# Performance work log

Measured on AMD Instinct MI355X. Metric: run time of the kernel, lower is better.

## Reference

```python
import jax, jax.numpy as jnp
import numpy as np


def setup_inputs() -> dict:
    key = jax.random.key(0)
    k1, k2, k3 = jax.random.split(key, 3)
    L, B, H = 256, 8, 512
    inputs = jax.random.normal(k1, (L, B, H), dtype=jnp.float32)
    attn_W = jax.random.normal(k2, (H, 2 * H), dtype=jnp.float32) * 0.02
    attn_b = jnp.zeros((H,), dtype=jnp.float32)
    score_W = jax.random.normal(k3, (1, H), dtype=jnp.float32) * 0.02
    score_b = jnp.zeros((1,), dtype=jnp.float32)
    return {"inputs": inputs, "attn_W": attn_W, "attn_b": attn_b,
            "score_W": score_W, "score_b": score_b}


def reference(inputs, attn_W, attn_b, score_W, score_b):
    # inputs: [L, B, H]; attn_W: [H, 2H] (torch Linear weight), attn_b: [H]
    # score_W: [1, H], score_b: [1]
    H = attn_W.shape[0]
    # Decompose Linear(cat(sen1, sen2)) = sen1 @ W1^T + sen2 @ W2^T + b
    W1 = attn_W[:, :H]   # [H, H] acts on sen1 (row index i)
    W2 = attn_W[:, H:]   # [H, H] acts on sen2 (col index j)
    x = jnp.transpose(inputs, (1, 0, 2))          # [B, L, H]
    p1 = jnp.einsum('blh,oh->blo', x, W1)         # [B, L, H]
    p2 = jnp.einsum('blh,oh->blo', x, W2)         # [B, L, H]
    # feat[b,i,j,:] = tanh(attn(cat(x[b,i], x[b,j])))  -> [B, L, L, H]
    feat = jnp.tanh(p1[:, :, None, :] + p2[:, None, :, :] + attn_b)
    # score Linear H -> 1, squeeze last dim -> [B, L, L]
    energies = jnp.einsum('bijh,h->bij', feat, score_W[0]) + score_b[0]
    # softmax over dim=1 (the sen1 / i axis), as in the torch code
    return jax.nn.softmax(energies, axis=1)
```

## Files before the change

kernel.cpp:

```cpp
#include <hip/hip_runtime.h>

#define LOG2E 1.4426950408889634f
#define SCALE (2.0f * LOG2E)

__device__ __forceinline__ float fast_exp2(float x) { return __builtin_amdgcn_exp2f(x); }
__device__ __forceinline__ float fast_rcp(float x)  { return __builtin_amdgcn_rcpf(x); }

typedef __attribute__((ext_vector_type(8))) short bf16x8;
typedef __attribute__((ext_vector_type(4))) float f32x4;

__global__ __launch_bounds__(256) void pack_kernel(const float* __restrict__ inputs,
                                                   const float* __restrict__ attn_W,
                                                   ushort* __restrict__ Ap,
                                                   ushort* __restrict__ Bp) {
    __shared__ ushort Hs[64 * 136];
    __shared__ ushort Ls[64 * 136];

    const int bid = blockIdx.x;
    const bool isA = bid < 128;
    const int sub = isA ? bid : bid - 128;
    const int tb = sub >> 2;
    const int kc = sub & 3;
    const int t = threadIdx.x;

#pragma unroll
    for (int it = 0; it < 4; ++it) {
        const int u = it * 256 + t;
        const int row = u >> 4;
        const int kc8 = u & 15;
        const float* src;
        if (isA) {
            int sr = ((tb & 3) * 64 + row) * 8 + (tb >> 2);
            src = inputs + (long)sr * 512 + kc * 128 + kc8 * 8;
        } else {
            int r = (tb & 7) * 64 + row;
            src = attn_W + (long)r * 1024 + (tb >> 3) * 512 + kc * 128 + kc8 * 8;
        }
        float4 v0 = *(const float4*)src;
        float4 v1 = *(const float4*)(src + 4);
        float vv[8] = {v0.x, v0.y, v0.z, v0.w, v1.x, v1.y, v1.z, v1.w};
        ushort hi8[8], lo8[8];
#pragma unroll
        for (int j = 0; j < 8; ++j) {
            unsigned u32 = __float_as_uint(vv[j]);
            unsigned h = (u32 + 0x7FFF + ((u32 >> 16) & 1)) >> 16;
            hi8[j] = (ushort)h;
            float lo = vv[j] - __uint_as_float(h << 16);
            unsigned ul = __float_as_uint(lo);
            lo8[j] = (ushort)((ul + 0x7FFF + ((ul >> 16) & 1)) >> 16);
        }
        const int lidx = row * 136 + kc8 * 8;
        *(uint4*)&Hs[lidx] = *(const uint4*)hi8;
        *(uint4*)&Ls[lidx] = *(const uint4*)lo8;
    }
    __syncthreads();

    ushort* P = (isA ? Ap : Bp) + (long)tb * 98304;
#pragma unroll
    for (int it = 0; it < 4; ++it) {
        const int u = it * 256 + t;
        const int l  = u & 63;
        const int fr = (u >> 6) & 3;
        const int ks = (u >> 8) & 1;
        const int ktl = (u >> 9) & 1;
        const int j = fr * 16 + (l & 15);
        const int klocal = ktl * 64 + ks * 32 + (l >> 4) * 8;
        uint4 h  = *(const uint4*)&Hs[j * 136 + klocal];
        uint4 lo = *(const uint4*)&Ls[j * 136 + klocal];
        const int kt0 = kc * 2 + ktl;
        const long off = (long)ks * 2048 + fr * 512 + l * 8;
        if (isA) {
            *(uint4*)(P + (kt0 +  0) * 4096 + off) = h;
            *(uint4*)(P + (kt0 + 16) * 4096 + off) = h;
            *(uint4*)(P + (kt0 +  8) * 4096 + off) = lo;
        } else {
            *(uint4*)(P + (kt0 +  0) * 4096 + off) = h;
            *(uint4*)(P + (kt0 +  8) * 4096 + off) = h;
            *(uint4*)(P + (kt0 + 16) * 4096 + off) = lo;
        }
    }
}

__global__ __launch_bounds__(512) void mfma_gemm(const ushort* __restrict__ Ap,
                                                 const ushort* __restrict__ Bp,
                                                 const float* __restrict__ attn_b,
                                                 float* __restrict__ E1,
                                                 float* __restrict__ E2) {
    const int xcd = blockIdx.x & 7;
    const int idx = blockIdx.x >> 3;
    const int mb  = xcd * 2 + (idx >> 4);
    const int nb  = idx & 15;
    __shared__ ushort lds[2][12288];

    const int t = threadIdx.x;
    const int lane = t & 63, w = t >> 6;
    const int wr = w >> 1, wc = w & 1;

    const ushort* A0 = Ap + (long)(mb * 2 + 0) * 98304;
    const ushort* A1 = Ap + (long)(mb * 2 + 1) * 98304;
    const ushort* B0 = Bp + (long)nb * 98304;

    f32x4 acc[2][2];
#pragma unroll
    for (int i = 0; i < 2; ++i)
#pragma unroll
        for (int j = 0; j < 2; ++j)
            acc[i][j] = (f32x4){0.f, 0.f, 0.f, 0.f};

    uint4 st[3];
#define LOADK(kt)                                                  \
    {                                                              \
        st[0] = ((const uint4*)(A0 + (kt) * 4096))[t];             \
        st[1] = ((const uint4*)(A1 + (kt) * 4096))[t];             \
        st[2] = ((const uint4*)(B0 + (kt) * 4096))[t];             \
    }
#define STOREK(bf)                                                 \
    {                                                              \
        uint4* d = (uint4*)lds[bf];                                \
        d[t] = st[0]; d[t + 512] = st[1]; d[t + 1024] = st[2];     \
    }

    LOADK(0);
    STOREK(0);
    __syncthreads();

    for (int kt = 0; kt < 24; ++kt) {
        if (kt < 23) LOADK(kt + 1);
        const ushort* buf = lds[kt & 1];
#pragma unroll
        for (int ks = 0; ks < 2; ++ks) {
            bf16x8 a[2], b[2];
            const int abase = (wr >> 1) * 4096 + ks * 2048 + (wr & 1) * 1024 + lane * 8;
            const int bbase = 8192 + ks * 2048 + wc * 1024 + lane * 8;
            a[0] = *(const bf16x8*)&buf[abase];
            a[1] = *(const bf16x8*)&buf[abase + 512];
            b[0] = *(const bf16x8*)&buf[bbase];
            b[1] = *(const bf16x8*)&buf[bbase + 512];
#pragma unroll
            for (int mf = 0; mf < 2; ++mf)
#pragma unroll
                for (int nf = 0; nf < 2; ++nf)
                    acc[mf][nf] = __builtin_amdgcn_mfma_f32_16x16x32_bf16(
                        a[mf], b[nf], acc[mf][nf], 0, 0, 0);
        }
        if (kt < 23) {
            STOREK((kt + 1) & 1);
            __syncthreads();
        }
    }
#undef LOADK
#undef STOREK

#pragma unroll
    for (int nf = 0; nf < 2; ++nf) {
        int n = nb * 64 + wc * 32 + nf * 16 + (lane & 15);
        const bool isE1 = (n < 512);
        float* dst = isE1 ? E1 : E2;
        int o = n & 511;
        float bias = isE1 ? attn_b[o] : 0.0f;
#pragma unroll
        for (int mf = 0; mf < 2; ++mf) {
            int ml = mb * 128 + wr * 32 + mf * 16 + ((lane >> 4) << 2);
            int bb = ml >> 8, l = ml & 255;
            long rowoff = ((long)(bb * 8 + (l >> 5)) * 512 + o) * 32 + (l & 31);
#pragma unroll
            for (int r = 0; r < 4; ++r)
                dst[rowoff + r] = fast_exp2(SCALE * (acc[mf][nf][r] + bias));
        }
    }
}

__global__ __launch_bounds__(256) void energy_kernel(const float* __restrict__ E1,
                                                     const float* __restrict__ E2,
                                                     const float* __restrict__ sW,
                                                     float* __restrict__ EP) {
    const int bid = blockIdx.x;
    const int tj = bid & 3;
    const int ti = (bid >> 2) & 3;
    const int b  = (bid >> 4) & 7;
    const int s  = bid >> 7;
    __shared__ float As[32 * 64];
    __shared__ float Bs[32 * 64];
    __shared__ float csh[128];

    const int t = threadIdx.x;
    const int tx = t & 15, ty = t >> 4;

    if (t < 128) csh[t] = 2.0f * sW[s * 128 + t];

    const float* e1base = E1 + (long)(b * 8 + ti * 2) * 16384;
    const float* e2base = E2 + (long)(b * 8 + tj * 2) * 16384;

    float acc[4][4];
#pragma unroll
    for (int i = 0; i < 4; ++i)
#pragma unroll
        for (int j = 0; j < 4; ++j) acc[i][j] = 0.f;

    for (int c0 = 0; c0 < 128; c0 += 32) {
        __syncthreads();
#pragma unroll
        for (int it = 0; it < 2; ++it) {
            const int f = it * 256 + t;
            const int ol = f >> 4;
            const int i4 = (f & 15) * 4;
            const long srcoff = (long)(i4 >> 5) * 16384 + (long)(s * 128 + c0 + ol) * 32 + (i4 & 31);
            *(float4*)&As[ol * 64 + i4] = *(const float4*)(e1base + srcoff);
            *(float4*)&Bs[ol * 64 + i4] = *(const float4*)(e2base + srcoff);
        }
        __syncthreads();

#pragma unroll 2
        for (int p = 0; p < 8; ++p) {
            const float4 c4 = *(const float4*)&csh[c0 + p * 4];
            float4 a0 = *(const float4*)&As[(p * 4 + 0) * 64 + ty * 4];
            float4 a1 = *(const float4*)&As[(p * 4 + 1) * 64 + ty * 4];
            float4 a2 = *(const float4*)&As[(p * 4 + 2) * 64 + ty * 4];
            float4 a3 = *(const float4*)&As[(p * 4 + 3) * 64 + ty * 4];
            float4 b0 = *(const float4*)&Bs[(p * 4 + 0) * 64 + tx * 4];
            float4 b1 = *(const float4*)&Bs[(p * 4 + 1) * 64 + tx * 4];
            float4 b2 = *(const float4*)&Bs[(p * 4 + 2) * 64 + tx * 4];
            float4 b3 = *(const float4*)&Bs[(p * 4 + 3) * 64 + tx * 4];
            const float a0v[4] = {a0.x, a0.y, a0.z, a0.w};
            const float a1v[4] = {a1.x, a1.y, a1.z, a1.w};
            const float a2v[4] = {a2.x, a2.y, a2.z, a2.w};
            const float a3v[4] = {a3.x, a3.y, a3.z, a3.w};
            const float b0v[4] = {b0.x, b0.y, b0.z, b0.w};
            const float b1v[4] = {b1.x, b1.y, b1.z, b1.w};
            const float b2v[4] = {b2.x, b2.y, b2.z, b2.w};
            const float b3v[4] = {b3.x, b3.y, b3.z, b3.w};
#pragma unroll
            for (int i = 0; i < 4; ++i) {
#pragma unroll
                for (int j = 0; j < 4; ++j) {
                    float y0 = fmaf(a0v[i], b0v[j], 1.0f);
                    float y1 = fmaf(a1v[i], b1v[j], 1.0f);
                    float y2 = fmaf(a2v[i], b2v[j], 1.0f);
                    float y3 = fmaf(a3v[i], b3v[j], 1.0f);
                    float y01 = y0 * y1, y23 = y2 * y3;
                    float d = y01 * y23;
                    float n01 = fmaf(c4.x, y1, c4.y * y0);
                    float n23 = fmaf(c4.z, y3, c4.w * y2);
                    float n = fmaf(n01, y23, n23 * y01);
                    acc[i][j] = fmaf(n, fast_rcp(d), acc[i][j]);
                }
            }
        }
    }

    float* Eb = EP + (long)s * 524288 + (long)b * 65536 +
                (long)(ti * 64 + ty * 4) * 256 + tj * 64 + tx * 4;
#pragma unroll
    for (int i = 0; i < 4; ++i)
        *(float4*)&Eb[i * 256] = make_float4(acc[i][0], acc[i][1], acc[i][2], acc[i][3]);
}

__global__ __launch_bounds__(256) void softmax_kernel(const float* __restrict__ P0,
                                                      const float* __restrict__ P1,
                                                      const float* __restrict__ P2,
                                                      const float* __restrict__ P3,
                                                      float* __restrict__ out) {
    const int b  = blockIdx.x >> 4;
    const int jt = blockIdx.x & 15;
    const int t  = threadIdx.x;
    const int jx = t & 15;
    const int iy = t >> 4;
    const long base = (long)b * 65536 + jt * 16 + jx;

    float v[16];
#pragma unroll
    for (int k = 0; k < 16; ++k) {
        long idx = base + (long)(iy + k * 16) * 256;
        v[k] = -(P0[idx] + P1[idx] + P2[idx] + P3[idx]);
    }

    float m = v[0];
#pragma unroll
    for (int k = 1; k < 16; ++k) m = fmaxf(m, v[k]);

    __shared__ float red[256];
    red[t] = m;
    __syncthreads();
    if (t < 128) red[t] = fmaxf(red[t], red[t + 128]);
    __syncthreads();
    if (t < 64) red[t] = fmaxf(red[t], red[t + 64]);
    __syncthreads();
    if (t < 32) red[t] = fmaxf(red[t], red[t + 32]);
    __syncthreads();
    if (t < 16) red[t] = fmaxf(red[t], red[t + 16]);
    __syncthreads();
    m = red[jx];
    __syncthreads();

    float ssum = 0.f;
#pragma unroll
    for (int k = 0; k < 16; ++k) {
        v[k] = fast_exp2((v[k] - m) * LOG2E);
        ssum += v[k];
    }
    red[t] = ssum;
    __syncthreads();
    if (t < 128) red[t] += red[t + 128];
    __syncthreads();
    if (t < 64) red[t] += red[t + 64];
    __syncthreads();
    if (t < 32) red[t] += red[t + 32];
    __syncthreads();
    if (t < 16) red[t] += red[t + 16];
    __syncthreads();
    float inv = fast_rcp(red[jx]);

#pragma unroll
    for (int k = 0; k < 16; ++k) {
        long idx = base + (long)(iy + k * 16) * 256;
        out[idx] = v[k] * inv;
    }
}

extern "C" void kernel_launch(void* const* d_in, const int* in_sizes, int n_in,
                              void* d_out, int out_size, void* d_ws, size_t ws_size,
                              hipStream_t stream) {
    const float* inputs  = (const float*)d_in[0];
    const float* attn_W  = (const float*)d_in[1];
    const float* attn_b  = (const float*)d_in[2];
    const float* score_W = (const float*)d_in[3];
    float* out = (float*)d_out;

    float* ws = (float*)d_ws;
    float* E1 = ws;
    float* E2 = ws + (1 << 20);
    float* EP = ws + (2 << 20);
    ushort* Ap = (ushort*)(ws + (4 << 20));
    ushort* Bp = Ap + 3145728;

    pack_kernel<<<192, 256, 0, stream>>>(inputs, attn_W, Ap, Bp);
    mfma_gemm<<<256, 512, 0, stream>>>(Ap, Bp, attn_b, E1, E2);
    energy_kernel<<<512, 256, 0, stream>>>(E1, E2, score_W, EP);
    softmax_kernel<<<128, 256, 0, stream>>>(EP, EP + 524288, EP + 2 * 524288,
                                            EP + 3 * 524288, out);
}
```

Measured before the change: 57.40 us.

## Fuse bf16 hi/lo split-packing into the MFMA GEMM and drop pack kernel

Removes the separate pack kernel, which wrote pre-split bf16 hi/lo operand tiles to workspace. The GEMM now loads fp32 inputs and weights directly, splits each value into hi and lo bf16 parts in registers, and writes them to LDS in MFMA layout. It then runs three MFMA passes per K stage (hi*hi, lo*hi, hi*lo). This saves one kernel launch and the packed-buffer write and read, at the cost of conversion work repeated by every block that reuses the same tile, and a single LDS buffer with two barriers per stage instead of double buffering.

Result: faster. 53.42 us (-6.9%).

```diff
diff --git a/kernel.cpp b/kernel.cpp
--- a/kernel.cpp
+++ b/kernel.cpp
@@ -9,80 +9,20 @@
 typedef __attribute__((ext_vector_type(8))) short bf16x8;
 typedef __attribute__((ext_vector_type(4))) float f32x4;
 
-__global__ __launch_bounds__(256) void pack_kernel(const float* __restrict__ inputs,
-                                                   const float* __restrict__ attn_W,
-                                                   ushort* __restrict__ Ap,
-                                                   ushort* __restrict__ Bp) {
-    __shared__ ushort Hs[64 * 136];
-    __shared__ ushort Ls[64 * 136];
-
-    const int bid = blockIdx.x;
-    const bool isA = bid < 128;
-    const int sub = isA ? bid : bid - 128;
-    const int tb = sub >> 2;
-    const int kc = sub & 3;
-    const int t = threadIdx.x;
-
-#pragma unroll
-    for (int it = 0; it < 4; ++it) {
-        const int u = it * 256 + t;
-        const int row = u >> 4;
-        const int kc8 = u & 15;
-        const float* src;
-        if (isA) {
-            int sr = ((tb & 3) * 64 + row) * 8 + (tb >> 2);
-            src = inputs + (long)sr * 512 + kc * 128 + kc8 * 8;
-        } else {
-            int r = (tb & 7) * 64 + row;
-            src = attn_W + (long)r * 1024 + (tb >> 3) * 512 + kc * 128 + kc8 * 8;
-        }
-        float4 v0 = *(const float4*)src;
-        float4 v1 = *(const float4*)(src + 4);
-        float vv[8] = {v0.x, v0.y, v0.z, v0.w, v1.x, v1.y, v1.z, v1.w};
-        ushort hi8[8], lo8[8];
-#pragma unroll
-        for (int j = 0; j < 8; ++j) {
-            unsigned u32 = __float_as_uint(vv[j]);
-            unsigned h = (u32 + 0x7FFF + ((u32 >> 16) & 1)) >> 16;
-            hi8[j] = (ushort)h;
-            float lo = vv[j] - __uint_as_float(h << 16);
-            unsigned ul = __float_as_uint(lo);
-            lo8[j] = (ushort)((ul + 0x7FFF + ((ul >> 16) & 1)) >> 16);
-        }
-        const int lidx = row * 136 + kc8 * 8;
-        *(uint4*)&Hs[lidx] = *(const uint4*)hi8;
-        *(uint4*)&Ls[lidx] = *(const uint4*)lo8;
-    }
-    __syncthreads();
-
-    ushort* P = (isA ? Ap : Bp) + (long)tb * 98304;
-#pragma unroll
-    for (int it = 0; it < 4; ++it) {
-        const int u = it * 256 + t;
-        const int l  = u & 63;
-        const int fr = (u >> 6) & 3;
-        const int ks = (u >> 8) & 1;
-        const int ktl = (u >> 9) & 1;
-        const int j = fr * 16 + (l & 15);
-        const int klocal = ktl * 64 + ks * 32 + (l >> 4) * 8;
-        uint4 h  = *(const uint4*)&Hs[j * 136 + klocal];
-        uint4 lo = *(const uint4*)&Ls[j * 136 + klocal];
-        const int kt0 = kc * 2 + ktl;
-        const long off = (long)ks * 2048 + fr * 512 + l * 8;
-        if (isA) {
-            *(uint4*)(P + (kt0 +  0) * 4096 + off) = h;
-            *(uint4*)(P + (kt0 + 16) * 4096 + off) = h;
-            *(uint4*)(P + (kt0 +  8) * 4096 + off) = lo;
-        } else {
-            *(uint4*)(P + (kt0 +  0) * 4096 + off) = h;
-            *(uint4*)(P + (kt0 +  8) * 4096 + off) = h;
-            *(uint4*)(P + (kt0 + 16) * 4096 + off) = lo;
-        }
-    }
-}
-
-__global__ __launch_bounds__(512) void mfma_gemm(const ushort* __restrict__ Ap,
-                                                 const ushort* __restrict__ Bp,
+__device__ __forceinline__ void cvt_hilo8(const float* vv, ushort* hi8, ushort* lo8) {
+#pragma unroll
+    for (int j = 0; j < 8; ++j) {
+        unsigned u32 = __float_as_uint(vv[j]);
+        unsigned h = (u32 + 0x7FFF + ((u32 >> 16) & 1)) >> 16;
+        hi8[j] = (ushort)h;
+        float lo = vv[j] - __uint_as_float(h << 16);
+        unsigned ul = __float_as_uint(lo);
+        lo8[j] = (ushort)((ul + 0x7FFF + ((ul >> 16) & 1)) >> 16);
+    }
+}
+
+__global__ __launch_bounds__(512) void mfma_gemm(const float* __restrict__ inputs,
+                                                 const float* __restrict__ attn_W,
                                                  const float* __restrict__ attn_b,
                                                  float* __restrict__ E1,
                                                  float* __restrict__ E2) {
@@ -90,15 +30,32 @@
     const int idx = blockIdx.x >> 3;
     const int mb  = xcd * 2 + (idx >> 4);
     const int nb  = idx & 15;
-    __shared__ ushort lds[2][12288];
+    __shared__ ushort lds[24576];
+    ushort* const Ahi = lds;
+    ushort* const Alo = lds + 8192;
+    ushort* const Bhi = lds + 16384;
+    ushort* const Blo = lds + 20480;
 
     const int t = threadIdx.x;
     const int lane = t & 63, w = t >> 6;
     const int wr = w >> 1, wc = w & 1;
 
-    const ushort* A0 = Ap + (long)(mb * 2 + 0) * 98304;
-    const ushort* A1 = Ap + (long)(mb * 2 + 1) * 98304;
-    const ushort* B0 = Bp + (long)nb * 98304;
+    const int arow0 = t >> 3, ak8 = t & 7;
+    const int arow1 = (t + 512) >> 3;
+    const int m0 = mb * 128 + arow0;
+    const int m1 = mb * 128 + arow1;
+    const float* asrc0 = inputs + (long)((m0 & 255) * 8 + (m0 >> 8)) * 512 + ak8 * 8;
+    const float* asrc1 = inputs + (long)((m1 & 255) * 8 + (m1 >> 8)) * 512 + ak8 * 8;
+    const int nloc = t >> 3, bk8 = t & 7;
+    const int ngl = nb * 64 + nloc;
+    const float* bsrc = attn_W + (long)(ngl & 511) * 1024 + (ngl >> 9) * 512 + bk8 * 8;
+
+    const int aoff0 = (arow0 >> 6) * 4096 + (ak8 >> 2) * 2048 + ((arow0 & 63) >> 4) * 512 +
+                      ((ak8 & 3) * 16 + (arow0 & 15)) * 8;
+    const int aoff1 = (arow1 >> 6) * 4096 + (ak8 >> 2) * 2048 + ((arow1 & 63) >> 4) * 512 +
+                      ((ak8 & 3) * 16 + (arow1 & 15)) * 8;
+    const int boff  = (bk8 >> 2) * 2048 + (nloc >> 4) * 512 +
+                      ((bk8 & 3) * 16 + (nloc & 15)) * 8;
 
     f32x4 acc[2][2];
 #pragma unroll
@@ -107,49 +64,59 @@
         for (int j = 0; j < 2; ++j)
             acc[i][j] = (f32x4){0.f, 0.f, 0.f, 0.f};
 
-    uint4 st[3];
-#define LOADK(kt)                                                  \
-    {                                                              \
-        st[0] = ((const uint4*)(A0 + (kt) * 4096))[t];             \
-        st[1] = ((const uint4*)(A1 + (kt) * 4096))[t];             \
-        st[2] = ((const uint4*)(B0 + (kt) * 4096))[t];             \
-    }
-#define STOREK(bf)                                                 \
-    {                                                              \
-        uint4* d = (uint4*)lds[bf];                                \
-        d[t] = st[0]; d[t + 512] = st[1]; d[t + 1024] = st[2];     \
-    }
-
-    LOADK(0);
-    STOREK(0);
-    __syncthreads();
-
-    for (int kt = 0; kt < 24; ++kt) {
-        if (kt < 23) LOADK(kt + 1);
-        const ushort* buf = lds[kt & 1];
-#pragma unroll
-        for (int ks = 0; ks < 2; ++ks) {
-            bf16x8 a[2], b[2];
-            const int abase = (wr >> 1) * 4096 + ks * 2048 + (wr & 1) * 1024 + lane * 8;
-            const int bbase = 8192 + ks * 2048 + wc * 1024 + lane * 8;
-            a[0] = *(const bf16x8*)&buf[abase];
-            a[1] = *(const bf16x8*)&buf[abase + 512];
-            b[0] = *(const bf16x8*)&buf[bbase];
-            b[1] = *(const bf16x8*)&buf[bbase + 512];
-#pragma unroll
-            for (int mf = 0; mf < 2; ++mf)
-#pragma unroll
-                for (int nf = 0; nf < 2; ++nf)
-                    acc[mf][nf] = __builtin_amdgcn_mfma_f32_16x16x32_bf16(
-                        a[mf], b[nf], acc[mf][nf], 0, 0, 0);
-        }
-        if (kt < 23) {
-            STOREK((kt + 1) & 1);
-            __syncthreads();
-        }
-    }
-#undef LOADK
-#undef STOREK
+    float ra0[8], ra1[8], rb[8];
+#define LOADF(ss)                                                              \
+    {                                                                          \
+        *(float4*)&ra0[0] = *(const float4*)(asrc0 + (ss) * 64);               \
+        *(float4*)&ra0[4] = *(const float4*)(asrc0 + (ss) * 64 + 4);           \
+        *(float4*)&ra1[0] = *(const float4*)(asrc1 + (ss) * 64);               \
+        *(float4*)&ra1[4] = *(const float4*)(asrc1 + (ss) * 64 + 4);           \
+        *(float4*)&rb[0]  = *(const float4*)(bsrc  + (ss) * 64);               \
+        *(float4*)&rb[4]  = *(const float4*)(bsrc  + (ss) * 64 + 4);           \
+    }
+
+    LOADF(0);
+
+    for (int ss = 0; ss < 8; ++ss) {
+        __syncthreads();
+        {
+            ushort h8[8], l8[8];
+            cvt_hilo8(ra0, h8, l8);
+            *(uint4*)&Ahi[aoff0] = *(const uint4*)h8;
+            *(uint4*)&Alo[aoff0] = *(const uint4*)l8;
+            cvt_hilo8(ra1, h8, l8);
+            *(uint4*)&Ahi[aoff1] = *(const uint4*)h8;
+            *(uint4*)&Alo[aoff1] = *(const uint4*)l8;
+            cvt_hilo8(rb, h8, l8);
+            *(uint4*)&Bhi[boff] = *(const uint4*)h8;
+            *(uint4*)&Blo[boff] = *(const uint4*)l8;
+        }
+        if (ss < 7) LOADF(ss + 1);
+        __syncthreads();
+
+#pragma unroll
+        for (int pass = 0; pass < 3; ++pass) {
+            const ushort* Ab = (pass == 1) ? Alo : Ahi;
+            const ushort* Bb = (pass == 2) ? Blo : Bhi;
+#pragma unroll
+            for (int ks = 0; ks < 2; ++ks) {
+                bf16x8 a[2], b[2];
+                const int abase = (wr >> 1) * 4096 + ks * 2048 + (wr & 1) * 1024 + lane * 8;
+                const int bbase = ks * 2048 + wc * 1024 + lane * 8;
+                a[0] = *(const bf16x8*)&Ab[abase];
+                a[1] = *(const bf16x8*)&Ab[abase + 512];
+                b[0] = *(const bf16x8*)&Bb[bbase];
+                b[1] = *(const bf16x8*)&Bb[bbase + 512];
+#pragma unroll
+                for (int mf = 0; mf < 2; ++mf)
+#pragma unroll
+                    for (int nf = 0; nf < 2; ++nf)
+                        acc[mf][nf] = __builtin_amdgcn_mfma_f32_16x16x32_bf16(
+                            a[mf], b[nf], acc[mf][nf], 0, 0, 0);
+            }
+        }
+    }
+#undef LOADF
 
 #pragma unroll
     for (int nf = 0; nf < 2; ++nf) {
@@ -330,11 +297,8 @@
     float* E1 = ws;
     float* E2 = ws + (1 << 20);
     float* EP = ws + (2 << 20);
-    ushort* Ap = (ushort*)(ws + (4 << 20));
-    ushort* Bp = Ap + 3145728;
-
-    pack_kernel<<<192, 256, 0, stream>>>(inputs, attn_W, Ap, Bp);
-    mfma_gemm<<<256, 512, 0, stream>>>(Ap, Bp, attn_b, E1, E2);
+
+    mfma_gemm<<<256, 512, 0, stream>>>(inputs, attn_W, attn_b, E1, E2);
     energy_kernel<<<512, 256, 0, stream>>>(E1, E2, score_W, EP);
     softmax_kernel<<<128, 256, 0, stream>>>(EP, EP + 524288, EP + 2 * 524288,
                                             EP + 3 * 524288, out);
```
